# Optimization experiments

Measured on AMD Instinct MI355X. Metric: run time of the kernel, lower is better.

The kernel has to match this reference:

```python
import jax, jax.numpy as jnp
import numpy as np

ALPHA = 0.2

def _ema_last_weights(T, alpha, dtype):
    # Closed form for the final EMA value after the sequential recurrence:
    # ema_T = (1-a)^(T-1) * x_0 + sum_{t=1}^{T-1} a*(1-a)^(T-1-t) * x_t
    t = jnp.arange(T)
    w = alpha * (1.0 - alpha) ** (T - 1 - t)
    w = w.at[0].set((1.0 - alpha) ** (T - 1))
    return w.astype(dtype)


def setup_inputs() -> dict:
    key = jax.random.key(0)
    k1, k2 = jax.random.split(key)
    B, T, F = 64, 2048, 256
    x = jax.random.normal(k1, (B, T, F), dtype=jnp.float32)
    W = jax.random.normal(k2, (F, F), dtype=jnp.float32) * (1.0 / np.sqrt(F))
    b = jnp.zeros((F,), dtype=jnp.float32)
    return {"x": x, "W": W, "b": b}


def reference(x, W, b):
    B, T, F = x.shape
    # final-step EMA over time (equivalent to the sequential python loop)
    w = _ema_last_weights(T, ALPHA, x.dtype)          # [T]
    last_ref = jnp.einsum('t,btf->bf', w, x)[:, None, :]  # [B,1,F]
    # base residual predictor: per-timestep linear
    res = jnp.einsum('btf,fg->btg', x, W) + b          # [B,T,F]
    return last_ref + res
```

## Files before the change

### kernel.cpp

```cpp
#include <hip/hip_runtime.h>
#include <hip/hip_bf16.h>

#define Bdim 64
#define Tdim 2048
#define Fdim 256
#define TAIL 256
#define NCH 8
#define CHT 32

#define BM 64
#define ASTR 264

typedef __bf16 bf16x8 __attribute__((ext_vector_type(8)));
typedef float f32x16 __attribute__((ext_vector_type(16)));
typedef unsigned short u16x8 __attribute__((ext_vector_type(8)));

__device__ __forceinline__ unsigned short bf16_rne(float f) {
  unsigned int u = __float_as_uint(f);
  u += 0x7FFFu + ((u >> 16) & 1u);
  return (unsigned short)(u >> 16);
}

__global__ void prep(const float* __restrict__ x, const float* __restrict__ W,
                     unsigned short* __restrict__ Wt, float* __restrict__ part) {
  if (blockIdx.x >= 512) {
    int base = (blockIdx.x - 512) * 1024 + threadIdx.x * 4;
#pragma unroll
    for (int j = 0; j < 4; ++j) {
      int i = base + j;
      int g = i >> 8, f = i & 255;
      Wt[i] = bf16_rne(W[f * Fdim + g]);
    }
    return;
  }
  int b = blockIdx.x & 63, c = blockIdx.x >> 6, f = threadIdx.x;
  int t0 = Tdim - TAIL + c * CHT;
  float w = 0.2f * exp2f((float)(Tdim - 1 - t0) * -0.32192809488736235f);
  const float* xp = x + ((size_t)b * Tdim + t0) * Fdim + f;
  float s = 0.f;
#pragma unroll
  for (int j = 0; j < CHT; ++j) {
    s += w * xp[(size_t)j * Fdim];
    w *= 1.25f;
  }
  part[(c * Bdim + b) * Fdim + f] = s;
}

__global__ __launch_bounds__(256, 3)
void gemm_fused(const float* __restrict__ x, const unsigned short* __restrict__ Wt,
                const float* __restrict__ bias, const float* __restrict__ part,
                float* __restrict__ out) {
  __shared__ unsigned short Abuf[BM * ASTR];

  const int tid = threadIdx.x;
  const int blk = blockIdx.x;
  const int b = blk >> 5;
  const size_t row0 = (size_t)blk * BM;

  const int wave = tid >> 6;
  const int lane = tid & 63;
  const int lm = lane & 31;
  const int half = lane >> 5;
  const int n0 = wave * 64 + lm;
  const int n1 = n0 + 32;

  float lb0 = bias[n0], lb1 = bias[n1];
#pragma unroll
  for (int c = 0; c < NCH; ++c) {
    lb0 += part[(c * Bdim + b) * Fdim + n0];
    lb1 += part[(c * Bdim + b) * Fdim + n1];
  }

  {
    const int r = tid >> 2;
    const int c0 = (tid & 3) * 64;
    const float4* src = (const float4*)&x[(row0 + r) * Fdim + c0];
#pragma unroll
    for (int i = 0; i < 8; ++i) {
      float4 v0 = src[2 * i];
      float4 v1 = src[2 * i + 1];
      u16x8 w;
      w[0] = bf16_rne(v0.x); w[1] = bf16_rne(v0.y);
      w[2] = bf16_rne(v0.z); w[3] = bf16_rne(v0.w);
      w[4] = bf16_rne(v1.x); w[5] = bf16_rne(v1.y);
      w[6] = bf16_rne(v1.z); w[7] = bf16_rne(v1.w);
      *(u16x8*)&Abuf[r * ASTR + c0 + i * 8] = w;
    }
  }
  __syncthreads();

  f32x16 acc[2][2] = {};
  const int ko = half * 8;

#pragma unroll 4
  for (int s = 0; s < 16; ++s) {
    const int kk = s * 16 + ko;
    bf16x8 a0 = *(const bf16x8*)&Abuf[lm * ASTR + kk];
    bf16x8 a1 = *(const bf16x8*)&Abuf[(32 + lm) * ASTR + kk];
    bf16x8 b0 = *(const bf16x8*)&Wt[(size_t)n0 * Fdim + kk];
    bf16x8 b1 = *(const bf16x8*)&Wt[(size_t)n1 * Fdim + kk];
    acc[0][0] = __builtin_amdgcn_mfma_f32_32x32x16_bf16(a0, b0, acc[0][0], 0, 0, 0);
    acc[0][1] = __builtin_amdgcn_mfma_f32_32x32x16_bf16(a0, b1, acc[0][1], 0, 0, 0);
    acc[1][0] = __builtin_amdgcn_mfma_f32_32x32x16_bf16(a1, b0, acc[1][0], 0, 0, 0);
    acc[1][1] = __builtin_amdgcn_mfma_f32_32x32x16_bf16(a1, b1, acc[1][1], 0, 0, 0);
  }

  float* op = out + row0 * Fdim;
  const int rbase = 4 * half;
#pragma unroll
  for (int i = 0; i < 2; ++i) {
#pragma unroll
    for (int j = 0; j < 2; ++j) {
      const int n = (j == 0) ? n0 : n1;
      const float lb = (j == 0) ? lb0 : lb1;
#pragma unroll
      for (int r = 0; r < 16; ++r) {
        int rowi = i * 32 + (r & 3) + 8 * (r >> 2) + rbase;
        op[(size_t)rowi * Fdim + n] = acc[i][j][r] + lb;
      }
    }
  }
}

extern "C" void kernel_launch(void* const* d_in, const int* in_sizes, int n_in,
                              void* d_out, int out_size, void* d_ws, size_t ws_size,
                              hipStream_t stream) {
  const float* x = (const float*)d_in[0];
  const float* W = (const float*)d_in[1];
  const float* bias = (const float*)d_in[2];
  float* out = (float*)d_out;

  unsigned short* Wt = (unsigned short*)d_ws;
  float* part = (float*)((char*)d_ws + Fdim * Fdim * sizeof(unsigned short));

  prep<<<576, 256, 0, stream>>>(x, W, Wt, part);
  gemm_fused<<<(Bdim * Tdim) / BM, 256, 0, stream>>>(x, Wt, bias, part, out);
}
```

Before: 271.9 us.

## Drop LDS staging of A and feed MFMA straight from global x

Removes the shared-memory tile and its barrier: each wave now loads its fp32 x rows straight from global memory and converts them to bf16 in registers right before each MFMA. The loop is fully unrolled and launch bounds are raised to target four blocks per CU. The aim is to cut LDS traffic, the synchronisation and the shared-memory footprint. The cost is that all four waves re-read and re-convert the same 64 rows, which adds L1/L2 traffic, and each load is a strided, narrowly coalesced access.

After: 311.2 us. 14.4% more time.

```diff
diff --git a/kernel.cpp b/kernel.cpp
--- a/kernel.cpp
+++ b/kernel.cpp
@@ -7,9 +7,7 @@
 #define TAIL 256
 #define NCH 8
 #define CHT 32
-
 #define BM 64
-#define ASTR 264
 
 typedef __bf16 bf16x8 __attribute__((ext_vector_type(8)));
 typedef float f32x16 __attribute__((ext_vector_type(16)));
@@ -19,6 +17,15 @@
   unsigned int u = __float_as_uint(f);
   u += 0x7FFFu + ((u >> 16) & 1u);
   return (unsigned short)(u >> 16);
+}
+
+__device__ __forceinline__ bf16x8 cvt8(float4 v0, float4 v1) {
+  u16x8 w;
+  w[0] = bf16_rne(v0.x); w[1] = bf16_rne(v0.y);
+  w[2] = bf16_rne(v0.z); w[3] = bf16_rne(v0.w);
+  w[4] = bf16_rne(v1.x); w[5] = bf16_rne(v1.y);
+  w[6] = bf16_rne(v1.z); w[7] = bf16_rne(v1.w);
+  return *(bf16x8*)&w;
 }
 
 __global__ void prep(const float* __restrict__ x, const float* __restrict__ W,
@@ -46,12 +53,10 @@
   part[(c * Bdim + b) * Fdim + f] = s;
 }
 
-__global__ __launch_bounds__(256, 3)
+__global__ __launch_bounds__(256, 4)
 void gemm_fused(const float* __restrict__ x, const unsigned short* __restrict__ Wt,
                 const float* __restrict__ bias, const float* __restrict__ part,
                 float* __restrict__ out) {
-  __shared__ unsigned short Abuf[BM * ASTR];
-
   const int tid = threadIdx.x;
   const int blk = blockIdx.x;
   const int b = blk >> 5;
@@ -71,34 +76,23 @@
     lb1 += part[(c * Bdim + b) * Fdim + n1];
   }
 
-  {
-    const int r = tid >> 2;
-    const int c0 = (tid & 3) * 64;
-    const float4* src = (const float4*)&x[(row0 + r) * Fdim + c0];
-#pragma unroll
-    for (int i = 0; i < 8; ++i) {
-      float4 v0 = src[2 * i];
-      float4 v1 = src[2 * i + 1];
-      u16x8 w;
-      w[0] = bf16_rne(v0.x); w[1] = bf16_rne(v0.y);
-      w[2] = bf16_rne(v0.z); w[3] = bf16_rne(v0.w);
-      w[4] = bf16_rne(v1.x); w[5] = bf16_rne(v1.y);
-      w[6] = bf16_rne(v1.z); w[7] = bf16_rne(v1.w);
-      *(u16x8*)&Abuf[r * ASTR + c0 + i * 8] = w;
-    }
-  }
-  __syncthreads();
+  const float4* ax0 = (const float4*)&x[(row0 + lm) * Fdim + half * 8];
+  const float4* ax1 = (const float4*)&x[(row0 + 32 + lm) * Fdim + half * 8];
+  const u16x8* bw0 = (const u16x8*)&Wt[(size_t)n0 * Fdim + half * 8];
+  const u16x8* bw1 = (const u16x8*)&Wt[(size_t)n1 * Fdim + half * 8];
 
   f32x16 acc[2][2] = {};
-  const int ko = half * 8;
 
-#pragma unroll 4
+#pragma unroll
   for (int s = 0; s < 16; ++s) {
-    const int kk = s * 16 + ko;
-    bf16x8 a0 = *(const bf16x8*)&Abuf[lm * ASTR + kk];
-    bf16x8 a1 = *(const bf16x8*)&Abuf[(32 + lm) * ASTR + kk];
-    bf16x8 b0 = *(const bf16x8*)&Wt[(size_t)n0 * Fdim + kk];
-    bf16x8 b1 = *(const bf16x8*)&Wt[(size_t)n1 * Fdim + kk];
+    float4 a0l = ax0[s * 4], a0h = ax0[s * 4 + 1];
+    float4 a1l = ax1[s * 4], a1h = ax1[s * 4 + 1];
+    u16x8 ub0 = bw0[s * 2];
+    u16x8 ub1 = bw1[s * 2];
+    bf16x8 a0 = cvt8(a0l, a0h);
+    bf16x8 a1 = cvt8(a1l, a1h);
+    bf16x8 b0 = *(bf16x8*)&ub0;
+    bf16x8 b1 = *(bf16x8*)&ub1;
     acc[0][0] = __builtin_amdgcn_mfma_f32_32x32x16_bf16(a0, b0, acc[0][0], 0, 0, 0);
     acc[0][1] = __builtin_amdgcn_mfma_f32_32x32x16_bf16(a0, b1, acc[0][1], 0, 0, 0);
     acc[1][0] = __builtin_amdgcn_mfma_f32_32x32x16_bf16(a1, b0, acc[1][0], 0, 0, 0);
```
